# Kernel optimization log

Measured on AMD Instinct MI355X. Metric: run time of the kernel, lower is better.

The kernel has to match this reference:

```python
import jax, jax.numpy as jnp
import numpy as np

B, N, P = 8, 64, 128
DNODE, DEDGE, DEMB = 2048, 1024, 512
E = B * N * N


def setup_inputs() -> dict:
    key = jax.random.key(0)
    ks = jax.random.split(key, 12)
    x = jax.random.normal(ks[0], (B, N, DNODE), dtype=jnp.float32)
    interaction_feature = jax.random.normal(ks[1], (B, N, N, DEDGE), dtype=jnp.float32)
    s = 0.02
    W_phi = jax.random.normal(ks[2], (DNODE, DEMB), dtype=jnp.float32) * s
    b_phi = jax.random.normal(ks[3], (DEMB,), dtype=jnp.float32) * s
    W_psi = jax.random.normal(ks[4], (DNODE, DEMB), dtype=jnp.float32) * s
    b_psi = jax.random.normal(ks[5], (DEMB,), dtype=jnp.float32) * s
    W_node = jax.random.normal(ks[6], (DNODE, DEMB), dtype=jnp.float32) * s
    b_node = jax.random.normal(ks[7], (DEMB,), dtype=jnp.float32) * s
    W_rel = jax.random.normal(ks[8], (DEDGE, DEMB), dtype=jnp.float32) * s
    b_rel = jax.random.normal(ks[9], (DEMB,), dtype=jnp.float32) * s
    pairs = jax.random.randint(ks[10], (B, P, 2), 0, N, dtype=jnp.int32)
    # edge_locating_tensor: rows (batch, src, dst) covering the proposed edge set
    bb, ii, jj = jnp.meshgrid(jnp.arange(B), jnp.arange(N), jnp.arange(N), indexing='ij')
    edge_locating_tensor = jnp.stack([bb.ravel(), ii.ravel(), jj.ravel()], axis=1).astype(jnp.int32)  # [E,3]
    return {"x": x, "interaction_feature": interaction_feature, "W_phi": W_phi, "b_phi": b_phi,
            "W_psi": W_psi, "b_psi": b_psi, "W_node": W_node, "b_node": b_node,
            "W_rel": W_rel, "b_rel": b_rel, "pairs": pairs, "edge_locating_tensor": edge_locating_tensor}


def _lookup_edge(elt, b_idx, i0, i1):
    # boolean-mask argmax lookup, faithful to torch argmax(loc0*loc1*loc2)
    # elt: [E,3]; b_idx,i0,i1: [B,P] -> loc: [B,P] indices into edge list
    m = (elt[None, None, :, 0] == b_idx[:, :, None]) \
        & (elt[None, None, :, 1] == i0[:, :, None]) \
        & (elt[None, None, :, 2] == i1[:, :, None])  # [B,P,E]
    return jnp.argmax(m, axis=-1)


def reference(x, interaction_feature, W_phi, b_phi, W_psi, b_psi,
              W_node, b_node, W_rel, b_rel, pairs, edge_locating_tensor):
    # relationship proposal scoring: all-pairs einsum + sigmoid
    phi = x @ W_phi + b_phi                                    # [B,N,512]
    psi = x @ W_psi + b_psi                                    # [B,N,512]
    relatedness_score = jax.nn.sigmoid(jnp.einsum('bik,bjk->bij', phi, psi))  # [B,N,N]

    # node / relationship-node embedders
    node_emb = x @ W_node + b_node                             # [B,N,512]
    elt = edge_locating_tensor
    rel_feats = interaction_feature[elt[:, 0], elt[:, 1], elt[:, 2]]  # [E,1024] gather
    edge_emb = rel_feats @ W_rel + b_rel                       # [E,512]

    # classifier input construction (gather/argmax/scatter hot path, vectorized)
    ind0, ind1 = pairs[..., 0], pairs[..., 1]                  # [B,P]
    b_idx = jnp.broadcast_to(jnp.arange(B, dtype=jnp.int32)[:, None], ind0.shape)
    emb0 = node_emb[b_idx, ind0]                               # [B,P,512]
    emb1 = node_emb[b_idx, ind1]
    first_half = (emb0 + emb1) * 0.5                           # aggregate 'mean'

    loc_fwd = _lookup_edge(elt, b_idx, ind0, ind1)             # [B,P]
    loc_rev = _lookup_edge(elt, b_idx, ind1, ind0)
    e1 = edge_emb[loc_fwd]                                     # [B,P,512]
    e2 = edge_emb[loc_rev]
    second_half = (e1 + e2) * 0.5

    classifier_input = jnp.concatenate([first_half, second_half], axis=-1)  # [B,P,1024]
    return relatedness_score, classifier_input
```

## Files before the change

kernel.cpp:

```cpp
#include <hip/hip_runtime.h>
#include <hip/hip_bf16.h>


typedef _Float16 h16;
typedef h16 h16x4 __attribute__((ext_vector_type(4)));
typedef h16 h16x8 __attribute__((ext_vector_type(8)));
typedef float f32x4 __attribute__((ext_vector_type(4)));


__global__ __launch_bounds__(256) void k_prep(
    const float* __restrict__ Wphi, const float* __restrict__ Wpsi,
    const float* __restrict__ Wnode, const float* __restrict__ Wrel,
    const float* __restrict__ x, const float* __restrict__ bphi,
    const float* __restrict__ bpsi, const float* __restrict__ bnode,
    const float* __restrict__ feat, const int* __restrict__ pairs,
    h16* __restrict__ W3t, h16* __restrict__ Wrelt, h16* __restrict__ xh,
    float* __restrict__ b3, h16* __restrict__ G) {
  __shared__ float t[32][33];
  int bid = blockIdx.x;
  if (bid < 3584) {
    const float* src; h16* dst; int K, tk, tn;
    if (bid < 3072) {
      int mat = bid >> 10, rem = bid & 1023;
      tk = rem >> 4; tn = rem & 15;
      src = mat == 0 ? Wphi : (mat == 1 ? Wpsi : Wnode);
      K = 2048; dst = W3t + (long)mat * 512 * 2048;
    } else {
      int rem = bid - 3072;
      tk = rem >> 4; tn = rem & 15;
      src = Wrel; K = 1024; dst = Wrelt;
    }
    int tx = threadIdx.x & 31, ty = threadIdx.x >> 5;
#pragma unroll
    for (int it = 0; it < 4; ++it)
      t[ty + it*8][tx] = src[(long)(tk*32 + ty + it*8)*512 + tn*32 + tx];
    __syncthreads();
#pragma unroll
    for (int it = 0; it < 4; ++it)
      dst[(long)(tn*32 + ty + it*8)*K + tk*32 + tx] = (h16)t[tx][ty + it*8];
  } else if (bid < 4102) {
    int b2 = bid - 3584;
    if (b2 < 512) {
      int idx = (b2*256 + threadIdx.x) * 8;
      const float4* xv = (const float4*)(x + idx);
      float4 v0 = xv[0], v1 = xv[1];
      h16x8 o;
      o[0]=(h16)v0.x; o[1]=(h16)v0.y; o[2]=(h16)v0.z; o[3]=(h16)v0.w;
      o[4]=(h16)v1.x; o[5]=(h16)v1.y; o[6]=(h16)v1.z; o[7]=(h16)v1.w;
      *(h16x8*)(xh + idx) = o;
    } else {
      int i = (b2 - 512)*256 + threadIdx.x;
      if (i < 1536) b3[i] = i < 512 ? bphi[i] : (i < 1024 ? bpsi[i-512] : bnode[i-1024]);
    }
  } else {
    int r = bid - 4102;
    int b = r >> 7;
    int i0 = pairs[r*2], i1 = pairs[r*2+1];
    const float4* f0 = (const float4*)(feat + (long)((b*64 + i0)*64 + i1) * 1024);
    const float4* f1 = (const float4*)(feat + (long)((b*64 + i1)*64 + i0) * 1024);
    int k = threadIdx.x;
    float4 a = f0[k], c = f1[k];
    h16x4 o;
    o[0]=(h16)(0.5f*(a.x+c.x)); o[1]=(h16)(0.5f*(a.y+c.y));
    o[2]=(h16)(0.5f*(a.z+c.z)); o[3]=(h16)(0.5f*(a.w+c.w));
    *(h16x4*)(G + (long)r*1024 + k*4) = o;
  }
}

__device__ __forceinline__ void mfma_compute(
    const h16 (*__restrict__ As)[72], const h16 (*__restrict__ Bs)[72],
    int wm, int wn, int fr, int kg, f32x4 acc[2][2]) {
#pragma unroll
  for (int kc = 0; kc < 2; ++kc) {
    int kb = kc*32 + kg;
    h16x8 fa0 = *(const h16x8*)&As[wm*32 + fr][kb];
    h16x8 fa1 = *(const h16x8*)&As[wm*32 + 16 + fr][kb];
    h16x8 fb0 = *(const h16x8*)&Bs[wn*32 + fr][kb];
    h16x8 fb1 = *(const h16x8*)&Bs[wn*32 + 16 + fr][kb];
    acc[0][0] = __builtin_amdgcn_mfma_f32_16x16x32_f16(fa0, fb0, acc[0][0], 0,0,0);
    acc[0][1] = __builtin_amdgcn_mfma_f32_16x16x32_f16(fa0, fb1, acc[0][1], 0,0,0);
    acc[1][0] = __builtin_amdgcn_mfma_f32_16x16x32_f16(fa1, fb0, acc[1][0], 0,0,0);
    acc[1][1] = __builtin_amdgcn_mfma_f32_16x16x32_f16(fa1, fb1, acc[1][1], 0,0,0);
  }
}

#define GEMM_PIPELINE(Agp, Bgp, K)                                        \
  {                                                                       \
    h16x8 ra0 = *(const h16x8*)(Agp);                                     \
    h16x8 ra1 = *(const h16x8*)(Agp + 8);                                 \
    h16x8 rb0 = *(const h16x8*)(Bgp);                                     \
    h16x8 rb1 = *(const h16x8*)(Bgp + 8);                                 \
    *(h16x8*)&As[0][srow][skp]   = ra0;                                   \
    *(h16x8*)&As[0][srow][skp+8] = ra1;                                   \
    *(h16x8*)&Bs[0][srow][skp]   = rb0;                                   \
    *(h16x8*)&Bs[0][srow][skp+8] = rb1;                                   \
    __syncthreads();                                                      \
    int cur = 0;                                                          \
    for (int k0 = 64; k0 < (K); k0 += 64) {                               \
      ra0 = *(const h16x8*)(Agp + k0);                                    \
      ra1 = *(const h16x8*)(Agp + k0 + 8);                                \
      rb0 = *(const h16x8*)(Bgp + k0);                                    \
      rb1 = *(const h16x8*)(Bgp + k0 + 8);                                \
      mfma_compute(As[cur], Bs[cur], wm, wn, fr, kg, acc);                \
      int nxt = cur ^ 1;                                                  \
      *(h16x8*)&As[nxt][srow][skp]   = ra0;                               \
      *(h16x8*)&As[nxt][srow][skp+8] = ra1;                               \
      *(h16x8*)&Bs[nxt][srow][skp]   = rb0;                               \
      *(h16x8*)&Bs[nxt][srow][skp+8] = rb1;                               \
      __syncthreads();                                                    \
      cur = nxt;                                                          \
    }                                                                     \
    mfma_compute(As[cur], Bs[cur], wm, wn, fr, kg, acc);                  \
  }

__global__ __launch_bounds__(256) void k_gemm(
    const h16* __restrict__ A1, const h16* __restrict__ B1,
    const float* __restrict__ bias1, float* __restrict__ C1,
    h16* __restrict__ Yh,
    const h16* __restrict__ A2, const h16* __restrict__ B2,
    const float* __restrict__ bias2, float* __restrict__ C2) {
  __shared__ __align__(16) h16 As[2][64][72];
  __shared__ __align__(16) h16 Bs[2][64][72];
  int bid = blockIdx.x;
  const h16 *A, *Bt; const float* bias; float* C;
  int K, ldc, tileM, tileN;
  if (bid < 192) {
    A = A1; Bt = B1; bias = bias1; C = C1; K = 2048; ldc = 1536;
    tileM = (bid / 24) * 64; tileN = (bid % 24) * 64;
  } else {
    int r = bid - 192;
    A = A2; Bt = B2; bias = bias2; C = C2; K = 1024; ldc = 1024;
    tileM = (r / 8) * 64; tileN = (r % 8) * 64;
  }
  int tid = threadIdx.x, lane = tid & 63, wave = tid >> 6;
  int wm = wave >> 1, wn = wave & 1;
  int srow = tid >> 2, skp = (tid & 3) * 16;
  int fr = lane & 15, kg = (lane >> 4) * 8;
  const h16* Agp = A + (long)(tileM + srow) * K + skp;
  const h16* Bgp = Bt + (long)(tileN + srow) * K + skp;
  f32x4 acc[2][2] = {};
  GEMM_PIPELINE(Agp, Bgp, K);
  int r0 = 4 * (lane >> 4), c0 = lane & 15;
  bool wantYh = (bid < 192) && (tileN < 1024);
#pragma unroll
  for (int m = 0; m < 2; ++m)
#pragma unroll
    for (int n = 0; n < 2; ++n) {
      int row = tileM + wm*32 + m*16 + r0;
      int col = tileN + wn*32 + n*16 + c0;
      float bb = bias[col];
#pragma unroll
      for (int r = 0; r < 4; ++r) {
        float v = acc[m][n][r] + bb;
        C[(long)(row + r) * ldc + col] = v;
        if (wantYh) Yh[(long)(row + r) * 1024 + col] = (h16)v;
      }
    }
}

__global__ __launch_bounds__(256) void k_epilogue(
    const float* __restrict__ Y, const h16* __restrict__ Yh,
    const int* __restrict__ pairs, float* __restrict__ out) {
  __shared__ __align__(16) h16 As[2][64][72];
  __shared__ __align__(16) h16 Bs[2][64][72];
  int bid = blockIdx.x;
  if (bid < 8) {
    int tid = threadIdx.x, lane = tid & 63, wave = tid >> 6;
    int wm = wave >> 1, wn = wave & 1;
    int srow = tid >> 2, skp = (tid & 3) * 16;
    int fr = lane & 15, kg = (lane >> 4) * 8;
    const h16* Ab = Yh + (long)bid * 64 * 1024;
    const h16* Agp = Ab + (long)srow * 1024 + skp;
    const h16* Bgp = Ab + (long)srow * 1024 + 512 + skp;
    f32x4 acc[2][2] = {};
    GEMM_PIPELINE(Agp, Bgp, 512);
    int r0 = 4 * (lane >> 4), c0 = lane & 15;
    float* ob = out + (long)bid * 4096;
#pragma unroll
    for (int m = 0; m < 2; ++m)
#pragma unroll
      for (int n = 0; n < 2; ++n) {
        int row = wm*32 + m*16 + r0;
        int col = wn*32 + n*16 + c0;
#pragma unroll
        for (int r = 0; r < 4; ++r) {
          float s = acc[m][n][r];
          ob[(long)(row + r) * 64 + col] = 1.f / (1.f + expf(-s));
        }
      }
  } else {
    int r = bid - 8;
    int b = r >> 7;
    int i0 = pairs[r*2], i1 = pairs[r*2+1];
    const float* n0 = Y + (long)(b*64 + i0)*1536 + 1024;
    const float* n1 = Y + (long)(b*64 + i1)*1536 + 1024;
    float* o = out + 32768 + (long)r*1024;
    for (int c = threadIdx.x; c < 512; c += 256)
      o[c] = 0.5f*(n0[c] + n1[c]);
  }
}

extern "C" void kernel_launch(void* const* d_in, const int* in_sizes, int n_in,
                              void* d_out, int out_size, void* d_ws, size_t ws_size,
                              hipStream_t stream) {
  const float* x     = (const float*)d_in[0];
  const float* feat  = (const float*)d_in[1];
  const float* Wphi  = (const float*)d_in[2];
  const float* bphi  = (const float*)d_in[3];
  const float* Wpsi  = (const float*)d_in[4];
  const float* bpsi  = (const float*)d_in[5];
  const float* Wnode = (const float*)d_in[6];
  const float* bnode = (const float*)d_in[7];
  const float* Wrel  = (const float*)d_in[8];
  const float* brel  = (const float*)d_in[9];
  const int*   pairs = (const int*)d_in[10];
  float* out = (float*)d_out;
  char* ws = (char*)d_ws;

  h16*   xh    = (h16*)(ws + 0);
  h16*   W3t   = (h16*)(ws + 2097152);
  h16*   Wrelt = (h16*)(ws + 8388608);
  h16*   G     = (h16*)(ws + 9437184);
  float* b3    = (float*)(ws + 11534336);
  float* Y     = (float*)(ws + 11540480);
  h16*   Yh    = (h16*)(ws + 14686208);

  k_prep<<<dim3(5126), dim3(256), 0, stream>>>(
      Wphi, Wpsi, Wnode, Wrel, x, bphi, bpsi, bnode, feat, pairs,
      W3t, Wrelt, xh, b3, G);
  k_gemm<<<dim3(320), dim3(256), 0, stream>>>(
      xh, W3t, b3, Y, Yh,
      G, Wrelt, brel, out + 32768 + 512);
  k_epilogue<<<dim3(1032), dim3(256), 0, stream>>>(Y, Yh, pairs, out);
}
```

Measured before the change: 41.91 us.

## Fuse three kernels into one persistent kernel with grid barriers

Replaces the prep, GEMM and epilogue launches with a single 256-block persistent kernel that moves between phases using an atomic-counter grid barrier, reset by a memset before launch. Each block loops over several prep units, GEMM tiles and epilogue rows. The aim is to remove inter-kernel launch gaps and tail effects. In exchange it adds spin-wait barrier costs and per-block serialisation. Correctness depends on all 256 blocks being co-resident, which holds on a 256-CU GPU.

```diff
diff --git a/kernel.cpp b/kernel.cpp
--- a/kernel.cpp
+++ b/kernel.cpp
@@ -7,64 +7,24 @@
 typedef h16 h16x8 __attribute__((ext_vector_type(8)));
 typedef float f32x4 __attribute__((ext_vector_type(4)));
 
-
-__global__ __launch_bounds__(256) void k_prep(
-    const float* __restrict__ Wphi, const float* __restrict__ Wpsi,
-    const float* __restrict__ Wnode, const float* __restrict__ Wrel,
-    const float* __restrict__ x, const float* __restrict__ bphi,
-    const float* __restrict__ bpsi, const float* __restrict__ bnode,
-    const float* __restrict__ feat, const int* __restrict__ pairs,
-    h16* __restrict__ W3t, h16* __restrict__ Wrelt, h16* __restrict__ xh,
-    float* __restrict__ b3, h16* __restrict__ G) {
-  __shared__ float t[32][33];
-  int bid = blockIdx.x;
-  if (bid < 3584) {
-    const float* src; h16* dst; int K, tk, tn;
-    if (bid < 3072) {
-      int mat = bid >> 10, rem = bid & 1023;
-      tk = rem >> 4; tn = rem & 15;
-      src = mat == 0 ? Wphi : (mat == 1 ? Wpsi : Wnode);
-      K = 2048; dst = W3t + (long)mat * 512 * 2048;
-    } else {
-      int rem = bid - 3072;
-      tk = rem >> 4; tn = rem & 15;
-      src = Wrel; K = 1024; dst = Wrelt;
-    }
-    int tx = threadIdx.x & 31, ty = threadIdx.x >> 5;
-#pragma unroll
-    for (int it = 0; it < 4; ++it)
-      t[ty + it*8][tx] = src[(long)(tk*32 + ty + it*8)*512 + tn*32 + tx];
-    __syncthreads();
-#pragma unroll
-    for (int it = 0; it < 4; ++it)
-      dst[(long)(tn*32 + ty + it*8)*K + tk*32 + tx] = (h16)t[tx][ty + it*8];
-  } else if (bid < 4102) {
-    int b2 = bid - 3584;
-    if (b2 < 512) {
-      int idx = (b2*256 + threadIdx.x) * 8;
-      const float4* xv = (const float4*)(x + idx);
-      float4 v0 = xv[0], v1 = xv[1];
-      h16x8 o;
-      o[0]=(h16)v0.x; o[1]=(h16)v0.y; o[2]=(h16)v0.z; o[3]=(h16)v0.w;
-      o[4]=(h16)v1.x; o[5]=(h16)v1.y; o[6]=(h16)v1.z; o[7]=(h16)v1.w;
-      *(h16x8*)(xh + idx) = o;
-    } else {
-      int i = (b2 - 512)*256 + threadIdx.x;
-      if (i < 1536) b3[i] = i < 512 ? bphi[i] : (i < 1024 ? bpsi[i-512] : bnode[i-1024]);
-    }
-  } else {
-    int r = bid - 4102;
-    int b = r >> 7;
-    int i0 = pairs[r*2], i1 = pairs[r*2+1];
-    const float4* f0 = (const float4*)(feat + (long)((b*64 + i0)*64 + i1) * 1024);
-    const float4* f1 = (const float4*)(feat + (long)((b*64 + i1)*64 + i0) * 1024);
-    int k = threadIdx.x;
-    float4 a = f0[k], c = f1[k];
-    h16x4 o;
-    o[0]=(h16)(0.5f*(a.x+c.x)); o[1]=(h16)(0.5f*(a.y+c.y));
-    o[2]=(h16)(0.5f*(a.z+c.z)); o[3]=(h16)(0.5f*(a.w+c.w));
-    *(h16x4*)(G + (long)r*1024 + k*4) = o;
-  }
+static const long O_XH   = 0;
+static const long O_W3T  = 2097152;
+static const long O_WREL = 8388608;
+static const long O_G    = 9437184;
+static const long O_B3   = 11534336;
+static const long O_Y    = 11540480;
+static const long O_YH   = 14686208;
+static const long O_CNT  = 15734784;
+
+__device__ __forceinline__ void grid_barrier(unsigned* cnt, unsigned target) {
+  __syncthreads();
+  if (threadIdx.x == 0) {
+    __threadfence();
+    __hip_atomic_fetch_add(cnt, 1u, __ATOMIC_ACQ_REL, __HIP_MEMORY_SCOPE_AGENT);
+    while (__hip_atomic_load(cnt, __ATOMIC_ACQUIRE, __HIP_MEMORY_SCOPE_AGENT) < target)
+      __builtin_amdgcn_s_sleep(2);
+  }
+  __syncthreads();
 }
 
 __device__ __forceinline__ void mfma_compute(
@@ -113,62 +73,118 @@
     mfma_compute(As[cur], Bs[cur], wm, wn, fr, kg, acc);                  \
   }
 
-__global__ __launch_bounds__(256) void k_gemm(
-    const h16* __restrict__ A1, const h16* __restrict__ B1,
-    const float* __restrict__ bias1, float* __restrict__ C1,
-    h16* __restrict__ Yh,
-    const h16* __restrict__ A2, const h16* __restrict__ B2,
-    const float* __restrict__ bias2, float* __restrict__ C2) {
+__global__ __launch_bounds__(256, 1) void k_fused(
+    const float* __restrict__ x, const float* __restrict__ feat,
+    const float* __restrict__ Wphi, const float* __restrict__ bphi,
+    const float* __restrict__ Wpsi, const float* __restrict__ bpsi,
+    const float* __restrict__ Wnode, const float* __restrict__ bnode,
+    const float* __restrict__ Wrel, const float* __restrict__ brel,
+    const int* __restrict__ pairs, float* __restrict__ out,
+    h16* __restrict__ xh, h16* __restrict__ W3t, h16* __restrict__ Wrelt,
+    h16* __restrict__ G, float* __restrict__ b3, float* __restrict__ Y,
+    h16* __restrict__ Yh, unsigned* cnt) {
+  __shared__ float t[32][33];
   __shared__ __align__(16) h16 As[2][64][72];
   __shared__ __align__(16) h16 Bs[2][64][72];
-  int bid = blockIdx.x;
-  const h16 *A, *Bt; const float* bias; float* C;
-  int K, ldc, tileM, tileN;
-  if (bid < 192) {
-    A = A1; Bt = B1; bias = bias1; C = C1; K = 2048; ldc = 1536;
-    tileM = (bid / 24) * 64; tileN = (bid % 24) * 64;
-  } else {
-    int r = bid - 192;
-    A = A2; Bt = B2; bias = bias2; C = C2; K = 1024; ldc = 1024;
-    tileM = (r / 8) * 64; tileN = (r % 8) * 64;
-  }
-  int tid = threadIdx.x, lane = tid & 63, wave = tid >> 6;
+  int bid = blockIdx.x, tid = threadIdx.x;
+
+#pragma unroll 1
+  for (int u0 = 0; u0 < 14; ++u0) {
+    int u = bid * 14 + u0;
+    const float* src; h16* dst; int K, tk, tn;
+    if (u < 3072) {
+      int mat = u >> 10, rem = u & 1023;
+      tk = rem >> 4; tn = rem & 15;
+      src = mat == 0 ? Wphi : (mat == 1 ? Wpsi : Wnode);
+      K = 2048; dst = W3t + (long)mat * 512 * 2048;
+    } else {
+      int rem = u - 3072;
+      tk = rem >> 4; tn = rem & 15;
+      src = Wrel; K = 1024; dst = Wrelt;
+    }
+    int tx = tid & 31, ty = tid >> 5;
+#pragma unroll
+    for (int it = 0; it < 4; ++it)
+      t[ty + it*8][tx] = src[(long)(tk*32 + ty + it*8)*512 + tn*32 + tx];
+    __syncthreads();
+#pragma unroll
+    for (int it = 0; it < 4; ++it)
+      dst[(long)(tn*32 + ty + it*8)*K + tk*32 + tx] = (h16)t[tx][ty + it*8];
+    __syncthreads();
+  }
+#pragma unroll 1
+  for (int u0 = 0; u0 < 2; ++u0) {
+    int idx = ((bid*2 + u0)*256 + tid) * 8;
+    const float4* xv = (const float4*)(x + idx);
+    float4 v0 = xv[0], v1 = xv[1];
+    h16x8 o;
+    o[0]=(h16)v0.x; o[1]=(h16)v0.y; o[2]=(h16)v0.z; o[3]=(h16)v0.w;
+    o[4]=(h16)v1.x; o[5]=(h16)v1.y; o[6]=(h16)v1.z; o[7]=(h16)v1.w;
+    *(h16x8*)(xh + idx) = o;
+  }
+  if (bid < 6) {
+    int i = bid*256 + tid;
+    b3[i] = i < 512 ? bphi[i] : (i < 1024 ? bpsi[i-512] : bnode[i-1024]);
+  }
+#pragma unroll 1
+  for (int u0 = 0; u0 < 4; ++u0) {
+    int r = bid*4 + u0;
+    int b = r >> 7;
+    int i0 = pairs[r*2], i1 = pairs[r*2+1];
+    const float4* f0 = (const float4*)(feat + (long)((b*64 + i0)*64 + i1) * 1024);
+    const float4* f1 = (const float4*)(feat + (long)((b*64 + i1)*64 + i0) * 1024);
+    float4 a = f0[tid], c = f1[tid];
+    h16x4 o;
+    o[0]=(h16)(0.5f*(a.x+c.x)); o[1]=(h16)(0.5f*(a.y+c.y));
+    o[2]=(h16)(0.5f*(a.z+c.z)); o[3]=(h16)(0.5f*(a.w+c.w));
+    *(h16x4*)(G + (long)r*1024 + tid*4) = o;
+  }
+
+  grid_barrier(cnt, 256);
+
+  int lane = tid & 63, wave = tid >> 6;
   int wm = wave >> 1, wn = wave & 1;
   int srow = tid >> 2, skp = (tid & 3) * 16;
   int fr = lane & 15, kg = (lane >> 4) * 8;
-  const h16* Agp = A + (long)(tileM + srow) * K + skp;
-  const h16* Bgp = Bt + (long)(tileN + srow) * K + skp;
-  f32x4 acc[2][2] = {};
-  GEMM_PIPELINE(Agp, Bgp, K);
-  int r0 = 4 * (lane >> 4), c0 = lane & 15;
-  bool wantYh = (bid < 192) && (tileN < 1024);
-#pragma unroll
-  for (int m = 0; m < 2; ++m)
-#pragma unroll
-    for (int n = 0; n < 2; ++n) {
-      int row = tileM + wm*32 + m*16 + r0;
-      int col = tileN + wn*32 + n*16 + c0;
-      float bb = bias[col];
-#pragma unroll
-      for (int r = 0; r < 4; ++r) {
-        float v = acc[m][n][r] + bb;
-        C[(long)(row + r) * ldc + col] = v;
-        if (wantYh) Yh[(long)(row + r) * 1024 + col] = (h16)v;
+  int ntile = bid < 192 ? 1 : 2;
+#pragma unroll 1
+  for (int ti = 0; ti < ntile; ++ti) {
+    if (ti) __syncthreads();
+    const h16 *A, *Bt; const float* bias; float* C;
+    int K, ldc, tileM, tileN;
+    if (bid < 192) {
+      A = xh; Bt = W3t; bias = b3; C = Y; K = 2048; ldc = 1536;
+      tileM = (bid / 24) * 64; tileN = (bid % 24) * 64;
+    } else {
+      int e = (bid - 192) * 2 + ti;
+      A = G; Bt = Wrelt; bias = brel; C = out + 32768 + 512; K = 1024; ldc = 1024;
+      tileM = (e >> 3) * 64; tileN = (e & 7) * 64;
+    }
+    const h16* Agp = A + (long)(tileM + srow) * K + skp;
+    const h16* Bgp = Bt + (long)(tileN + srow) * K + skp;
+    f32x4 acc[2][2] = {};
+    GEMM_PIPELINE(Agp, Bgp, K);
+    int r0 = 4 * (lane >> 4), c0 = lane & 15;
+    bool wantYh = (bid < 192) && (tileN < 1024);
+#pragma unroll
+    for (int m = 0; m < 2; ++m)
+#pragma unroll
+      for (int n = 0; n < 2; ++n) {
+        int row = tileM + wm*32 + m*16 + r0;
+        int col = tileN + wn*32 + n*16 + c0;
+        float bb = bias[col];
+#pragma unroll
+        for (int r = 0; r < 4; ++r) {
+          float v = acc[m][n][r] + bb;
+          C[(long)(row + r) * ldc + col] = v;
+          if (wantYh) Yh[(long)(row + r) * 1024 + col] = (h16)v;
+        }
       }
-    }
-}
-
-__global__ __launch_bounds__(256) void k_epilogue(
-    const float* __restrict__ Y, const h16* __restrict__ Yh,
-    const int* __restrict__ pairs, float* __restrict__ out) {
-  __shared__ __align__(16) h16 As[2][64][72];
-  __shared__ __align__(16) h16 Bs[2][64][72];
-  int bid = blockIdx.x;
+  }
+
+  grid_barrier(cnt, 512);
+
   if (bid < 8) {
-    int tid = threadIdx.x, lane = tid & 63, wave = tid >> 6;
-    int wm = wave >> 1, wn = wave & 1;
-    int srow = tid >> 2, skp = (tid & 3) * 16;
-    int fr = lane & 15, kg = (lane >> 4) * 8;
     const h16* Ab = Yh + (long)bid * 64 * 1024;
     const h16* Agp = Ab + (long)srow * 1024 + skp;
     const h16* Bgp = Ab + (long)srow * 1024 + 512 + skp;
@@ -189,14 +205,16 @@
         }
       }
   } else {
-    int r = bid - 8;
-    int b = r >> 7;
-    int i0 = pairs[r*2], i1 = pairs[r*2+1];
-    const float* n0 = Y + (long)(b*64 + i0)*1536 + 1024;
-    const float* n1 = Y + (long)(b*64 + i1)*1536 + 1024;
-    float* o = out + 32768 + (long)r*1024;
-    for (int c = threadIdx.x; c < 512; c += 256)
-      o[c] = 0.5f*(n0[c] + n1[c]);
+#pragma unroll 1
+    for (int u = bid - 8; u < 1024; u += 248) {
+      int b = u >> 7;
+      int i0 = pairs[u*2], i1 = pairs[u*2+1];
+      const float* n0 = Y + (long)(b*64 + i0)*1536 + 1024;
+      const float* n1 = Y + (long)(b*64 + i1)*1536 + 1024;
+      float* o = out + 32768 + (long)u*1024;
+      for (int c = tid; c < 512; c += 256)
+        o[c] = 0.5f*(n0[c] + n1[c]);
+    }
   }
 }
 
@@ -217,19 +235,10 @@
   float* out = (float*)d_out;
   char* ws = (char*)d_ws;
 
-  h16*   xh    = (h16*)(ws + 0);
-  h16*   W3t   = (h16*)(ws + 2097152);
-  h16*   Wrelt = (h16*)(ws + 8388608);
-  h16*   G     = (h16*)(ws + 9437184);
-  float* b3    = (float*)(ws + 11534336);
-  float* Y     = (float*)(ws + 11540480);
-  h16*   Yh    = (h16*)(ws + 14686208);
-
-  k_prep<<<dim3(5126), dim3(256), 0, stream>>>(
-      Wphi, Wpsi, Wnode, Wrel, x, bphi, bpsi, bnode, feat, pairs,
-      W3t, Wrelt, xh, b3, G);
-  k_gemm<<<dim3(320), dim3(256), 0, stream>>>(
-      xh, W3t, b3, Y, Yh,
-      G, Wrelt, brel, out + 32768 + 512);
-  k_epilogue<<<dim3(1032), dim3(256), 0, stream>>>(Y, Yh, pairs, out);
-}
+  hipMemsetAsync(ws + O_CNT, 0, 4, stream);
+  k_fused<<<dim3(256), dim3(256), 0, stream>>>(
+      x, feat, Wphi, bphi, Wpsi, bpsi, Wnode, bnode, Wrel, brel, pairs, out,
+      (h16*)(ws + O_XH), (h16*)(ws + O_W3T), (h16*)(ws + O_WREL),
+      (h16*)(ws + O_G), (float*)(ws + O_B3), (float*)(ws + O_Y),
+      (h16*)(ws + O_YH), (unsigned*)(ws + O_CNT));
+}
```

Result: slower. 108.2 us (+158.1%).

## Fuse fp32-to-fp16 conversion, weight transpose and edge gather into GEMM loads

Applied to the files above, without the earlier changes.

Removes the separate prep kernel that transposed and converted weights and inputs to fp16 and gathered edge features. The GEMM now reads fp32 x, weights and paired edge features directly, averages the forward and reverse edge rows in registers, converts to fp16 and stores into LDS. Edge tiles are processed two per block so the grid has 256 blocks. This saves one launch and a round trip through global memory. In exchange, weight columns are read with 16 strided scalar loads per thread, and every tile re-reads and re-converts fp32 data.

```diff
diff --git a/kernel.cpp b/kernel.cpp
--- a/kernel.cpp
+++ b/kernel.cpp
@@ -7,65 +7,8 @@
 typedef h16 h16x8 __attribute__((ext_vector_type(8)));
 typedef float f32x4 __attribute__((ext_vector_type(4)));
 
-
-__global__ __launch_bounds__(256) void k_prep(
-    const float* __restrict__ Wphi, const float* __restrict__ Wpsi,
-    const float* __restrict__ Wnode, const float* __restrict__ Wrel,
-    const float* __restrict__ x, const float* __restrict__ bphi,
-    const float* __restrict__ bpsi, const float* __restrict__ bnode,
-    const float* __restrict__ feat, const int* __restrict__ pairs,
-    h16* __restrict__ W3t, h16* __restrict__ Wrelt, h16* __restrict__ xh,
-    float* __restrict__ b3, h16* __restrict__ G) {
-  __shared__ float t[32][33];
-  int bid = blockIdx.x;
-  if (bid < 3584) {
-    const float* src; h16* dst; int K, tk, tn;
-    if (bid < 3072) {
-      int mat = bid >> 10, rem = bid & 1023;
-      tk = rem >> 4; tn = rem & 15;
-      src = mat == 0 ? Wphi : (mat == 1 ? Wpsi : Wnode);
-      K = 2048; dst = W3t + (long)mat * 512 * 2048;
-    } else {
-      int rem = bid - 3072;
-      tk = rem >> 4; tn = rem & 15;
-      src = Wrel; K = 1024; dst = Wrelt;
-    }
-    int tx = threadIdx.x & 31, ty = threadIdx.x >> 5;
-#pragma unroll
-    for (int it = 0; it < 4; ++it)
-      t[ty + it*8][tx] = src[(long)(tk*32 + ty + it*8)*512 + tn*32 + tx];
-    __syncthreads();
-#pragma unroll
-    for (int it = 0; it < 4; ++it)
-      dst[(long)(tn*32 + ty + it*8)*K + tk*32 + tx] = (h16)t[tx][ty + it*8];
-  } else if (bid < 4102) {
-    int b2 = bid - 3584;
-    if (b2 < 512) {
-      int idx = (b2*256 + threadIdx.x) * 8;
-      const float4* xv = (const float4*)(x + idx);
-      float4 v0 = xv[0], v1 = xv[1];
-      h16x8 o;
-      o[0]=(h16)v0.x; o[1]=(h16)v0.y; o[2]=(h16)v0.z; o[3]=(h16)v0.w;
-      o[4]=(h16)v1.x; o[5]=(h16)v1.y; o[6]=(h16)v1.z; o[7]=(h16)v1.w;
-      *(h16x8*)(xh + idx) = o;
-    } else {
-      int i = (b2 - 512)*256 + threadIdx.x;
-      if (i < 1536) b3[i] = i < 512 ? bphi[i] : (i < 1024 ? bpsi[i-512] : bnode[i-1024]);
-    }
-  } else {
-    int r = bid - 4102;
-    int b = r >> 7;
-    int i0 = pairs[r*2], i1 = pairs[r*2+1];
-    const float4* f0 = (const float4*)(feat + (long)((b*64 + i0)*64 + i1) * 1024);
-    const float4* f1 = (const float4*)(feat + (long)((b*64 + i1)*64 + i0) * 1024);
-    int k = threadIdx.x;
-    float4 a = f0[k], c = f1[k];
-    h16x4 o;
-    o[0]=(h16)(0.5f*(a.x+c.x)); o[1]=(h16)(0.5f*(a.y+c.y));
-    o[2]=(h16)(0.5f*(a.z+c.z)); o[3]=(h16)(0.5f*(a.w+c.w));
-    *(h16x4*)(G + (long)r*1024 + k*4) = o;
-  }
-}
+static const long O_Y  = 0;
+static const long O_YH = 3145728;
 
 __device__ __forceinline__ void mfma_compute(
     const h16 (*__restrict__ As)[72], const h16 (*__restrict__ Bs)[72],
@@ -84,7 +27,124 @@
   }
 }
 
-#define GEMM_PIPELINE(Agp, Bgp, K)                                        \
+#define LD4(p) (*(const float4*)(p))
+
+#define LOADREGS(k0_)                                                     \
+  {                                                                       \
+    const float* pa = arow0 + (k0_) + kseg;                               \
+    a0_ = LD4(pa); a1_ = LD4(pa+4); a2_ = LD4(pa+8); a3_ = LD4(pa+12);    \
+    if (isEdge) {                                                         \
+      const float* pq = arow1 + (k0_) + kseg;                             \
+      float4 q0 = LD4(pq), q1 = LD4(pq+4), q2 = LD4(pq+8), q3 = LD4(pq+12);\
+      a0_.x=0.5f*(a0_.x+q0.x); a0_.y=0.5f*(a0_.y+q0.y); a0_.z=0.5f*(a0_.z+q0.z); a0_.w=0.5f*(a0_.w+q0.w); \
+      a1_.x=0.5f*(a1_.x+q1.x); a1_.y=0.5f*(a1_.y+q1.y); a1_.z=0.5f*(a1_.z+q1.z); a1_.w=0.5f*(a1_.w+q1.w); \
+      a2_.x=0.5f*(a2_.x+q2.x); a2_.y=0.5f*(a2_.y+q2.y); a2_.z=0.5f*(a2_.z+q2.z); a2_.w=0.5f*(a2_.w+q2.w); \
+      a3_.x=0.5f*(a3_.x+q3.x); a3_.y=0.5f*(a3_.y+q3.y); a3_.z=0.5f*(a3_.z+q3.z); a3_.w=0.5f*(a3_.w+q3.w); \
+    }                                                                     \
+    const float* pb = bcol + (long)((k0_) + kblk) * 512;                  \
+    _Pragma("unroll")                                                     \
+    for (int i = 0; i < 16; ++i) b_[i] = pb[(long)i * 512];               \
+  }
+
+#define WRITEREGS(bufi)                                                   \
+  {                                                                       \
+    h16x8 wa0, wa1;                                                       \
+    wa0[0]=(h16)a0_.x; wa0[1]=(h16)a0_.y; wa0[2]=(h16)a0_.z; wa0[3]=(h16)a0_.w; \
+    wa0[4]=(h16)a1_.x; wa0[5]=(h16)a1_.y; wa0[6]=(h16)a1_.z; wa0[7]=(h16)a1_.w; \
+    wa1[0]=(h16)a2_.x; wa1[1]=(h16)a2_.y; wa1[2]=(h16)a2_.z; wa1[3]=(h16)a2_.w; \
+    wa1[4]=(h16)a3_.x; wa1[5]=(h16)a3_.y; wa1[6]=(h16)a3_.z; wa1[7]=(h16)a3_.w; \
+    *(h16x8*)&As[bufi][srow][kseg]     = wa0;                             \
+    *(h16x8*)&As[bufi][srow][kseg + 8] = wa1;                             \
+    h16x8 wb0, wb1;                                                       \
+    wb0[0]=(h16)b_[0]; wb0[1]=(h16)b_[1]; wb0[2]=(h16)b_[2]; wb0[3]=(h16)b_[3]; \
+    wb0[4]=(h16)b_[4]; wb0[5]=(h16)b_[5]; wb0[6]=(h16)b_[6]; wb0[7]=(h16)b_[7]; \
+    wb1[0]=(h16)b_[8]; wb1[1]=(h16)b_[9]; wb1[2]=(h16)b_[10]; wb1[3]=(h16)b_[11]; \
+    wb1[4]=(h16)b_[12]; wb1[5]=(h16)b_[13]; wb1[6]=(h16)b_[14]; wb1[7]=(h16)b_[15]; \
+    *(h16x8*)&Bs[bufi][ncol][kblk]     = wb0;                             \
+    *(h16x8*)&Bs[bufi][ncol][kblk + 8] = wb1;                             \
+  }
+
+__global__ __launch_bounds__(256) void k_gemm(
+    const float* __restrict__ x, const float* __restrict__ feat,
+    const float* __restrict__ Wphi, const float* __restrict__ Wpsi,
+    const float* __restrict__ Wnode, const float* __restrict__ bphi,
+    const float* __restrict__ bpsi, const float* __restrict__ bnode,
+    const float* __restrict__ Wrel, const float* __restrict__ brel,
+    const int* __restrict__ pairs,
+    float* __restrict__ Y, h16* __restrict__ Yh, float* __restrict__ out) {
+  __shared__ __align__(16) h16 As[2][64][72];
+  __shared__ __align__(16) h16 Bs[2][64][72];
+  int bid = blockIdx.x, tid = threadIdx.x;
+  int lane = tid & 63, wave = tid >> 6;
+  int wm = wave >> 1, wn = wave & 1;
+  int srow = tid >> 2, kseg = (tid & 3) * 16;
+  int ncol = tid & 63, kblk = (tid >> 6) * 16;
+  int fr = lane & 15, kg = (lane >> 4) * 8;
+
+  int isEdge = bid >= 192;
+  int ntile = isEdge ? 2 : 1;
+#pragma unroll 1
+  for (int ti = 0; ti < ntile; ++ti) {
+    if (ti) __syncthreads();
+    int K, tileM, tileN;
+    const float *arow0, *arow1, *bcol;
+    if (!isEdge) {
+      K = 2048; tileM = (bid / 24) * 64; tileN = (bid % 24) * 64;
+      arow0 = arow1 = x + (long)(tileM + srow) * 2048;
+      int mat = tileN >> 9;
+      const float* Wm = mat == 0 ? Wphi : (mat == 1 ? Wpsi : Wnode);
+      bcol = Wm + (tileN & 511) + ncol;
+    } else {
+      int e = (bid - 192) * 2 + ti;
+      K = 1024; tileM = (e >> 3) * 64; tileN = (e & 7) * 64;
+      int r = tileM + srow, b = r >> 7;
+      int i0 = pairs[r*2], i1 = pairs[r*2+1];
+      arow0 = feat + (long)((b*64 + i0)*64 + i1) * 1024;
+      arow1 = feat + (long)((b*64 + i1)*64 + i0) * 1024;
+      bcol = Wrel + tileN + ncol;
+    }
+    float4 a0_, a1_, a2_, a3_; float b_[16];
+    f32x4 acc[2][2] = {};
+    LOADREGS(0)
+    WRITEREGS(0)
+    __syncthreads();
+    int cur = 0;
+#pragma unroll 1
+    for (int k0 = 64; k0 < K; k0 += 64) {
+      LOADREGS(k0)
+      mfma_compute(As[cur], Bs[cur], wm, wn, fr, kg, acc);
+      WRITEREGS(cur ^ 1)
+      __syncthreads();
+      cur ^= 1;
+    }
+    mfma_compute(As[cur], Bs[cur], wm, wn, fr, kg, acc);
+
+    int r0 = 4 * (lane >> 4), c0 = lane & 15;
+#pragma unroll
+    for (int m = 0; m < 2; ++m)
+#pragma unroll
+      for (int n = 0; n < 2; ++n) {
+        int row = tileM + wm*32 + m*16 + r0;
+        int col = tileN + wn*32 + n*16 + c0;
+        if (!isEdge) {
+          float bb = col < 512 ? bphi[col] : (col < 1024 ? bpsi[col-512] : bnode[col-1024]);
+#pragma unroll
+          for (int r = 0; r < 4; ++r) {
+            float v = acc[m][n][r] + bb;
+            Y[(long)(row + r) * 1536 + col] = v;
+            if (col < 1024) Yh[(long)(row + r) * 1024 + col] = (h16)v;
+          }
+        } else {
+          float bb = brel[col];
+#pragma unroll
+          for (int r = 0; r < 4; ++r)
+            out[32768 + 512 + (long)(row + r) * 1024 + col] = acc[m][n][r] + bb;
+        }
+      }
+  }
+}
+
+#define GEMM_PIPELINE_H16(Agp, Bgp, K)                                    \
   {                                                                       \
     h16x8 ra0 = *(const h16x8*)(Agp);                                     \
     h16x8 ra1 = *(const h16x8*)(Agp + 8);                                 \
@@ -113,59 +173,14 @@
     mfma_compute(As[cur], Bs[cur], wm, wn, fr, kg, acc);                  \
   }
 
-__global__ __launch_bounds__(256) void k_gemm(
-    const h16* __restrict__ A1, const h16* __restrict__ B1,
-    const float* __restrict__ bias1, float* __restrict__ C1,
-    h16* __restrict__ Yh,
-    const h16* __restrict__ A2, const h16* __restrict__ B2,
-    const float* __restrict__ bias2, float* __restrict__ C2) {
-  __shared__ __align__(16) h16 As[2][64][72];
-  __shared__ __align__(16) h16 Bs[2][64][72];
-  int bid = blockIdx.x;
-  const h16 *A, *Bt; const float* bias; float* C;
-  int K, ldc, tileM, tileN;
-  if (bid < 192) {
-    A = A1; Bt = B1; bias = bias1; C = C1; K = 2048; ldc = 1536;
-    tileM = (bid / 24) * 64; tileN = (bid % 24) * 64;
-  } else {
-    int r = bid - 192;
-    A = A2; Bt = B2; bias = bias2; C = C2; K = 1024; ldc = 1024;
-    tileM = (r / 8) * 64; tileN = (r % 8) * 64;
-  }
-  int tid = threadIdx.x, lane = tid & 63, wave = tid >> 6;
-  int wm = wave >> 1, wn = wave & 1;
-  int srow = tid >> 2, skp = (tid & 3) * 16;
-  int fr = lane & 15, kg = (lane >> 4) * 8;
-  const h16* Agp = A + (long)(tileM + srow) * K + skp;
-  const h16* Bgp = Bt + (long)(tileN + srow) * K + skp;
-  f32x4 acc[2][2] = {};
-  GEMM_PIPELINE(Agp, Bgp, K);
-  int r0 = 4 * (lane >> 4), c0 = lane & 15;
-  bool wantYh = (bid < 192) && (tileN < 1024);
-#pragma unroll
-  for (int m = 0; m < 2; ++m)
-#pragma unroll
-    for (int n = 0; n < 2; ++n) {
-      int row = tileM + wm*32 + m*16 + r0;
-      int col = tileN + wn*32 + n*16 + c0;
-      float bb = bias[col];
-#pragma unroll
-      for (int r = 0; r < 4; ++r) {
-        float v = acc[m][n][r] + bb;
-        C[(long)(row + r) * ldc + col] = v;
-        if (wantYh) Yh[(long)(row + r) * 1024 + col] = (h16)v;
-      }
-    }
-}
-
 __global__ __launch_bounds__(256) void k_epilogue(
     const float* __restrict__ Y, const h16* __restrict__ Yh,
     const int* __restrict__ pairs, float* __restrict__ out) {
   __shared__ __align__(16) h16 As[2][64][72];
   __shared__ __align__(16) h16 Bs[2][64][72];
-  int bid = blockIdx.x;
+  int bid = blockIdx.x, tid = threadIdx.x;
   if (bid < 8) {
-    int tid = threadIdx.x, lane = tid & 63, wave = tid >> 6;
+    int lane = tid & 63, wave = tid >> 6;
     int wm = wave >> 1, wn = wave & 1;
     int srow = tid >> 2, skp = (tid & 3) * 16;
     int fr = lane & 15, kg = (lane >> 4) * 8;
@@ -173,7 +188,7 @@
     const h16* Agp = Ab + (long)srow * 1024 + skp;
     const h16* Bgp = Ab + (long)srow * 1024 + 512 + skp;
     f32x4 acc[2][2] = {};
-    GEMM_PIPELINE(Agp, Bgp, 512);
+    GEMM_PIPELINE_H16(Agp, Bgp, 512);
     int r0 = 4 * (lane >> 4), c0 = lane & 15;
     float* ob = out + (long)bid * 4096;
 #pragma unroll
@@ -195,7 +210,7 @@
     const float* n0 = Y + (long)(b*64 + i0)*1536 + 1024;
     const float* n1 = Y + (long)(b*64 + i1)*1536 + 1024;
     float* o = out + 32768 + (long)r*1024;
-    for (int c = threadIdx.x; c < 512; c += 256)
+    for (int c = tid; c < 512; c += 256)
       o[c] = 0.5f*(n0[c] + n1[c]);
   }
 }
@@ -217,19 +232,11 @@
   float* out = (float*)d_out;
   char* ws = (char*)d_ws;
 
-  h16*   xh    = (h16*)(ws + 0);
-  h16*   W3t   = (h16*)(ws + 2097152);
-  h16*   Wrelt = (h16*)(ws + 8388608);
-  h16*   G     = (h16*)(ws + 9437184);
-  float* b3    = (float*)(ws + 11534336);
-  float* Y     = (float*)(ws + 11540480);
-  h16*   Yh    = (h16*)(ws + 14686208);
-
-  k_prep<<<dim3(5126), dim3(256), 0, stream>>>(
-      Wphi, Wpsi, Wnode, Wrel, x, bphi, bpsi, bnode, feat, pairs,
-      W3t, Wrelt, xh, b3, G);
-  k_gemm<<<dim3(320), dim3(256), 0, stream>>>(
-      xh, W3t, b3, Y, Yh,
-      G, Wrelt, brel, out + 32768 + 512);
+  float* Y  = (float*)(ws + O_Y);
+  h16*   Yh = (h16*)(ws + O_YH);
+
+  k_gemm<<<dim3(256), dim3(256), 0, stream>>>(
+      x, feat, Wphi, Wpsi, Wnode, bphi, bpsi, bnode, Wrel, brel, pairs,
+      Y, Yh, out);
   k_epilogue<<<dim3(1032), dim3(256), 0, stream>>>(Y, Yh, pairs, out);
 }
```

Result: slower. 58.86 us (+40.4%).
